# Kernel tuning notes

Hardware: AMD Instinct MI355X
Metric: run time of the kernel (lower is better)

## Reference

```python
import jax, jax.numpy as jnp
import numpy as np

# ---- static config (matches init_kwargs) ----
IMG = 56        # num_patches = image_size // patch_size = 112 // 2
WIN = 7         # window_size
SHIFT = 3       # shift_size
C = 256         # projection_dim
H = 8           # num_heads
DH = C // H     # head dim = 32
S = WIN * WIN   # tokens per window = 49
NY = IMG // WIN # windows per side = 8
NW = NY * NY    # windows per image = 64
NMLP = 1024
EPS = 1e-5
SCALE = DH ** (-0.5)


def _relative_position_index():
    ch, cw = np.meshgrid(np.arange(WIN), np.arange(WIN), indexing='ij')
    coords = np.stack([ch, cw]).reshape(2, -1)                 # [2, S]
    rel = coords[:, :, None] - coords[:, None, :]              # [2, S, S]
    rel = rel.transpose(1, 2, 0) + (WIN - 1)                   # [S, S, 2]
    idx = rel[:, :, 0] * (2 * WIN - 1) + rel[:, :, 1]          # [S, S]
    return idx.reshape(-1)                                     # [S*S]

REL_IDX = jnp.asarray(_relative_position_index(), dtype=jnp.int32)


def _attn_mask():
    # Faithful replication of the module's mask construction (incl. the empty
    h_slices = (slice(0, -WIN), slice(-WIN, -SHIFT), slice(-SHIFT, None))
    w_slices = (slice(0, -WIN), slice(-WIN, -WIN), slice(-SHIFT, None))
    m = np.zeros((IMG, IMG), dtype=np.float32)
    count = 0
    for hs in h_slices:
        for ws in w_slices:
            m[hs, ws] = count
            count += 1
    mw = m.reshape(NY, WIN, NY, WIN).transpose(0, 2, 1, 3).reshape(NW, S)
    diff = mw[:, None, :] - mw[:, :, None]
    return np.where(diff != 0, -100.0, 0.0).astype(np.float32)  # [NW, S, S]

ATTN_MASK = jnp.asarray(_attn_mask())


def _layernorm(x, gamma, beta):
    mu = jnp.mean(x, axis=-1, keepdims=True)
    var = jnp.mean(jnp.square(x - mu), axis=-1, keepdims=True)
    return (x - mu) * jax.lax.rsqrt(var + EPS) * gamma + beta


def setup_inputs() -> dict:
    key = jax.random.key(0)
    ks = jax.random.split(key, 12)
    B = 32
    s = lambda fan: 1.0 / np.sqrt(fan)
    return {
        'x': jax.random.normal(ks[0], (B, IMG * IMG, C), dtype=jnp.float32),
        'norm_gamma': jnp.ones((C,), jnp.float32),
        'norm_beta': jnp.zeros((C,), jnp.float32),
        'qkv_w': jax.random.normal(ks[1], (C, 3 * C), jnp.float32) * s(C),
        'qkv_b': jnp.zeros((3 * C,), jnp.float32),
        'proj_w': jax.random.normal(ks[2], (C, C), jnp.float32) * s(C),
        'proj_b': jnp.zeros((C,), jnp.float32),
        'rel_bias_table': jax.random.truncated_normal(ks[3], -2.0, 2.0, ((2 * WIN - 1) ** 2, H), jnp.float32) * 0.02,
        'mlp_w1': jax.random.normal(ks[4], (C, NMLP), jnp.float32) * s(C),
        'mlp_b1': jnp.zeros((NMLP,), jnp.float32),
        'mlp_w2': jax.random.normal(ks[5], (NMLP, C), jnp.float32) * s(NMLP),
        'mlp_b2': jnp.zeros((C,), jnp.float32),
    }


def reference(x, norm_gamma, norm_beta, qkv_w, qkv_b, proj_w, proj_b,
              rel_bias_table, mlp_w1, mlp_b1, mlp_w2, mlp_b2):
    B = x.shape[0]
    # ---- shifted-window attention block ----
    shortcut = x
    xn = _layernorm(x, norm_gamma, norm_beta).reshape(B, IMG, IMG, C)
    shifted = jnp.roll(xn, shift=(-SHIFT, -SHIFT), axis=(1, 2))
    # window partition -> [B*NW, S, C]
    xw = shifted.reshape(B, NY, WIN, NY, WIN, C).transpose(0, 1, 3, 2, 4, 5)
    xw = xw.reshape(B * NW, S, C)
    qkv = xw @ qkv_w + qkv_b                                    # [BnW, S, 3C]
    qkv = qkv.reshape(B * NW, S, 3, H, DH).transpose(2, 0, 3, 1, 4)
    q, k, v = qkv[0] * SCALE, qkv[1], qkv[2]                    # [BnW, H, S, DH]
    attn = jnp.einsum('whsd,whtd->whst', q, k)                  # [BnW, H, S, S]
    bias = rel_bias_table[REL_IDX].reshape(S, S, H).transpose(2, 0, 1)
    attn = attn + bias[None]
    attn = attn.reshape(B, NW, H, S, S) + ATTN_MASK[None, :, None]
    attn = jax.nn.softmax(attn.reshape(B * NW, H, S, S), axis=-1)
    out = jnp.einsum('whst,whtd->wshd', attn, v).reshape(B * NW, S, C)
    out = out @ proj_w + proj_b
    # window reverse + unshift
    out = out.reshape(B, NY, NY, WIN, WIN, C).transpose(0, 1, 3, 2, 4, 5)
    out = out.reshape(B, IMG, IMG, C)
    out = jnp.roll(out, shift=(SHIFT, SHIFT), axis=(1, 2)).reshape(B, IMG * IMG, C)
    x = shortcut + out
    # ---- MLP block (same LayerNorm weights reused, as in original) ----
    shortcut2 = x
    xn2 = _layernorm(x, norm_gamma, norm_beta)
    h = jax.nn.gelu(xn2 @ mlp_w1 + mlp_b1, approximate=False)
    h = h @ mlp_w2 + mlp_b2
    return shortcut2 + h
```

## Files before the change

kernel.cpp:

```cpp
#include <hip/hip_runtime.h>
#include <math.h>

#define IMG   56
#define WINSZ 7
#define SHIFTSZ 3
#define CDIM  256
#define NH    8
#define DH    32
#define SEQ   49
#define NYW   8
#define NWIN  64
#define NMLP  1024
#define BATCH 32
#define NTOK  (BATCH*IMG*IMG)
#define BNW   (BATCH*NWIN)
#define SZT   ((size_t)NTOK*CDIM)
#define QSCALE 0.17677669529663687f
#define EPSLN 1e-5f

typedef __attribute__((ext_vector_type(8))) short short8;
typedef __attribute__((ext_vector_type(4))) float f32x4;

__device__ __forceinline__ float bf2f(unsigned short u) {
    union { unsigned i; float f; } c; c.i = ((unsigned)u) << 16; return c.f;
}
__device__ __forceinline__ unsigned short f2bf(float f) {
    union { float f; unsigned i; } c; c.f = f;
    unsigned r = c.i + 0x7fffu + ((c.i >> 16) & 1u);
    return (unsigned short)(r >> 16);
}

#define GLL16(gp, lp) __builtin_amdgcn_global_load_lds( \
    (__attribute__((address_space(1))) void*)(gp),      \
    (__attribute__((address_space(3))) void*)(lp), 16, 0, 0)

__global__ __launch_bounds__(256) void wtrans(const float* __restrict__ in,
                                              unsigned short* __restrict__ out,
                                              int K, int N) {
    int idx = blockIdx.x * 256 + threadIdx.x;
    if (idx >= K * N) return;
    int n = idx / K, k = idx - n * K;
    out[idx] = f2bf(in[(size_t)k * N + n]);
}

template<int WINDOWED>
__global__ __launch_bounds__(256) void ln_kernel(const float* __restrict__ x,
                                                 const float* __restrict__ gamma,
                                                 const float* __restrict__ beta,
                                                 unsigned short* __restrict__ out) {
    int wave = threadIdx.x >> 6;
    int lane = threadIdx.x & 63;
    int tok  = blockIdx.x * 4 + wave;
    int src  = tok;
    if (WINDOWED) {
        int b  = tok / (NWIN * SEQ);
        int r  = tok - b * (NWIN * SEQ);
        int wl = r / SEQ, s = r - wl * SEQ;
        int wy = wl >> 3, wx = wl & 7;
        int i  = s / WINSZ, j = s - i * WINSZ;
        int hp = wy * WINSZ + i + SHIFTSZ; if (hp >= IMG) hp -= IMG;
        int wp = wx * WINSZ + j + SHIFTSZ; if (wp >= IMG) wp -= IMG;
        src = b * (IMG * IMG) + hp * IMG + wp;
    }
    float4 v = *(const float4*)(x + (size_t)src * CDIM + lane * 4);
    float sum = v.x + v.y + v.z + v.w;
    float ss  = v.x*v.x + v.y*v.y + v.z*v.z + v.w*v.w;
#pragma unroll
    for (int off = 32; off; off >>= 1) {
        sum += __shfl_xor(sum, off);
        ss  += __shfl_xor(ss,  off);
    }
    float mu   = sum * (1.0f / CDIM);
    float var  = ss * (1.0f / CDIM) - mu * mu;
    float rstd = rsqrtf(var + EPSLN);
    float4 g  = *(const float4*)(gamma + lane * 4);
    float4 be = *(const float4*)(beta  + lane * 4);
    ushort4 o;
    o.x = f2bf((v.x - mu) * rstd * g.x + be.x);
    o.y = f2bf((v.y - mu) * rstd * g.y + be.y);
    o.z = f2bf((v.z - mu) * rstd * g.z + be.z);
    o.w = f2bf((v.w - mu) * rstd * g.w + be.w);
    *(ushort4*)(out + (size_t)tok * CDIM + lane * 4) = o;
}

#define EPI_QKV  0
#define EPI_PROJ 1
#define EPI_MLP1 2
#define EPI_MLP2 3

template<int EPI>
__global__ __launch_bounds__(256)
void gemm_bt(const unsigned short* __restrict__ A,
             const unsigned short* __restrict__ Bt,
             int K,
             const float* __restrict__ bias,
             const float* __restrict__ resin,
             float* __restrict__ outF,
             unsigned short* __restrict__ outH) {
    __shared__ __align__(16) unsigned short As[128 * 32];
    __shared__ __align__(16) unsigned short Bs[128 * 32];
    int tid  = threadIdx.x;
    int lane = tid & 63, wave = tid >> 6;
    int q    = lane >> 4, l16 = lane & 15;
    int wm   = wave >> 1, wn = wave & 1;
    int rowBase = blockIdx.x * 128;
    int colBase = blockIdx.y * 128;

    f32x4 acc[4][4];
#pragma unroll
    for (int i = 0; i < 4; i++)
#pragma unroll
        for (int j = 0; j < 4; j++) acc[i][j] = (f32x4){0.f, 0.f, 0.f, 0.f};

    const unsigned short* Ab = A  + (size_t)rowBase * K;
    const unsigned short* Bb = Bt + (size_t)colBase * K;

    int r0 = wave * 32;
    int ra = r0 + (lane >> 2);
    int rb = ra + 16;
    int ca = (lane & 3) ^ ((ra >> 1) & 3);
    int cb = (lane & 3) ^ ((rb >> 1) & 3);
    const size_t off1 = (size_t)ra * K + ca * 8;
    const size_t off2 = (size_t)rb * K + cb * 8;
    unsigned short* ldsA1 = &As[r0 * 32];
    unsigned short* ldsA2 = &As[(r0 + 16) * 32];
    unsigned short* ldsB1 = &Bs[r0 * 32];
    unsigned short* ldsB2 = &Bs[(r0 + 16) * 32];

    for (int k0 = 0; k0 < K; k0 += 32) {
        __syncthreads();
        GLL16(Ab + off1 + k0, ldsA1);
        GLL16(Ab + off2 + k0, ldsA2);
        GLL16(Bb + off1 + k0, ldsB1);
        GLL16(Bb + off2 + k0, ldsB2);
        __syncthreads();
        short8 af[4], bf[4];
#pragma unroll
        for (int mi = 0; mi < 4; mi++) {
            int r = wm * 64 + mi * 16 + l16;
            af[mi] = *(const short8*)&As[r * 32 + ((q ^ ((r >> 1) & 3)) * 8)];
        }
#pragma unroll
        for (int ni = 0; ni < 4; ni++) {
            int r = wn * 64 + ni * 16 + l16;
            bf[ni] = *(const short8*)&Bs[r * 32 + ((q ^ ((r >> 1) & 3)) * 8)];
        }
#pragma unroll
        for (int mi = 0; mi < 4; mi++)
#pragma unroll
            for (int ni = 0; ni < 4; ni++)
                acc[mi][ni] = __builtin_amdgcn_mfma_f32_16x16x32_bf16(
                    af[mi], bf[ni], acc[mi][ni], 0, 0, 0);
    }

    int mb = rowBase + wm * 64;
    int nb = colBase + wn * 64;

    if (EPI == EPI_QKV) {
#pragma unroll
        for (int mi = 0; mi < 4; mi++)
#pragma unroll
            for (int r = 0; r < 4; r++) {
                int m = mb + mi * 16 + q * 4 + r;
                int w = m / SEQ, s = m - w * SEQ;
#pragma unroll
                for (int ni = 0; ni < 4; ni++) {
                    int n0 = nb + ni * 16 + l16;
                    int three = n0 >> 8, hh = (n0 >> 5) & 7, dd = n0 & 31;
                    float v = acc[mi][ni][r] + bias[n0];
                    if (three == 0) {
                        v *= QSCALE;
                        outH[(((size_t)w * NH + hh) * SEQ + s) * DH + dd] = f2bf(v);
                    } else if (three == 1) {
                        outH[SZT + (((size_t)w * NH + hh) * SEQ + s) * DH + dd] = f2bf(v);
                    } else {
                        outH[2 * SZT + (((size_t)w * NH + hh) * DH + dd) * 64 + s] = f2bf(v);
                    }
                }
            }
    } else if (EPI == EPI_PROJ) {
#pragma unroll
        for (int mi = 0; mi < 4; mi++)
#pragma unroll
            for (int r = 0; r < 4; r++) {
                int m = mb + mi * 16 + q * 4 + r;
                int w = m / SEQ, s = m - w * SEQ;
                int b = w >> 6, wl = w & 63;
                int wy = wl >> 3, wx = wl & 7;
                int ii = s / WINSZ, jj = s - ii * WINSZ;
                int hp = wy * WINSZ + ii + SHIFTSZ; if (hp >= IMG) hp -= IMG;
                int wp = wx * WINSZ + jj + SHIFTSZ; if (wp >= IMG) wp -= IMG;
                size_t tok = (size_t)b * (IMG * IMG) + hp * IMG + wp;
#pragma unroll
                for (int ni = 0; ni < 4; ni++) {
                    int n0 = nb + ni * 16 + l16;
                    outF[tok * CDIM + n0] = acc[mi][ni][r] + bias[n0] +
                                            resin[tok * CDIM + n0];
                }
            }
    } else if (EPI == EPI_MLP1) {
#pragma unroll
        for (int mi = 0; mi < 4; mi++)
#pragma unroll
            for (int r = 0; r < 4; r++) {
                int m = mb + mi * 16 + q * 4 + r;
#pragma unroll
                for (int ni = 0; ni < 4; ni++) {
                    int n0 = nb + ni * 16 + l16;
                    float t = acc[mi][ni][r] + bias[n0];
                    float g = 0.5f * t * (1.0f + erff(t * 0.70710678118654752f));
                    outH[(size_t)m * NMLP + n0] = f2bf(g);
                }
            }
    } else {
#pragma unroll
        for (int mi = 0; mi < 4; mi++)
#pragma unroll
            for (int r = 0; r < 4; r++) {
                int m = mb + mi * 16 + q * 4 + r;
#pragma unroll
                for (int ni = 0; ni < 4; ni++) {
                    int n0 = nb + ni * 16 + l16;
                    outF[(size_t)m * CDIM + n0] = acc[mi][ni][r] + bias[n0] +
                                                  resin[(size_t)m * CDIM + n0];
                }
            }
    }
}

__global__ __launch_bounds__(256) void attn_mfma(const unsigned short* __restrict__ qb,
                                                 const unsigned short* __restrict__ kb,
                                                 const unsigned short* __restrict__ vT,
                                                 const float* __restrict__ rel_tab,
                                                 unsigned short* __restrict__ outp) {
    __shared__ __align__(16) unsigned short Pl[4][64 * 64];
    __shared__ float tab[4][169];
    int tid  = threadIdx.x;
    int wave = tid >> 6, lane = tid & 63;
    int q4   = lane >> 4, l16 = lane & 15;
    int job  = blockIdx.x * 4 + wave;
    int w    = job >> 3, h = job & 7;

    for (int i = lane; i < 169; i += 64) tab[wave][i] = rel_tab[i * NH + h];

    const unsigned short* qg = qb + (size_t)(w * NH + h) * SEQ * DH;
    const unsigned short* kg = kb + (size_t)(w * NH + h) * SEQ * DH;
    short8 aq[4], bk[4];
#pragma unroll
    for (int mi = 0; mi < 4; mi++)
        aq[mi] = *(const short8*)(qg + (mi * 16 + l16) * DH + q4 * 8);
#pragma unroll
    for (int ni = 0; ni < 4; ni++)
        bk[ni] = *(const short8*)(kg + (ni * 16 + l16) * DH + q4 * 8);

    f32x4 acc[4][4];
#pragma unroll
    for (int i = 0; i < 4; i++)
#pragma unroll
        for (int j = 0; j < 4; j++) acc[i][j] = (f32x4){0.f, 0.f, 0.f, 0.f};
#pragma unroll
    for (int mi = 0; mi < 4; mi++)
#pragma unroll
        for (int ni = 0; ni < 4; ni++)
            acc[mi][ni] = __builtin_amdgcn_mfma_f32_16x16x32_bf16(
                aq[mi], bk[ni], acc[mi][ni], 0, 0, 0);

    int wl = w & 63;
    int wy = wl >> 3, wx = wl & 7;
    bool edge = (wy == 7) || (wx == 7);

    int itv[4], jtv[4], ltv[4];
#pragma unroll
    for (int ni = 0; ni < 4; ni++) {
        int t  = ni * 16 + l16;
        int it = (t * 37) >> 8;
        int jt = t - it * 7;
        itv[ni] = it; jtv[ni] = jt;
        int lab;
        if (wx == 7 && jt < 4) lab = 0;
        else {
            int lh = (wy == 7) ? ((it < 4) ? 1 : 2) : 0;
            lab = lh * 3 + ((wx == 7) ? 2 : 0);
        }
        ltv[ni] = lab;
    }

    float rinv[4][4];
#pragma unroll
    for (int mi = 0; mi < 4; mi++) {
#pragma unroll
        for (int r = 0; r < 4; r++) {
            int s  = mi * 16 + q4 * 4 + r;
            int is = (s * 37) >> 8;
            int js = s - is * 7;
            int lab_s;
            if (wx == 7 && js < 4) lab_s = 0;
            else {
                int lh = (wy == 7) ? ((is < 4) ? 1 : 2) : 0;
                lab_s = lh * 3 + ((wx == 7) ? 2 : 0);
            }
            float vv[4];
#pragma unroll
            for (int ni = 0; ni < 4; ni++) {
                int t = ni * 16 + l16;
                float a = acc[mi][ni][r];
                if (t < SEQ) {
                    int idx = (is - itv[ni] + 6) * 13 + (js - jtv[ni] + 6);
                    idx = idx < 0 ? 0 : (idx > 168 ? 168 : idx);
                    a += tab[wave][idx];
                    if (edge && lab_s != ltv[ni]) a -= 100.0f;
                } else {
                    a = -1e30f;
                }
                vv[ni] = a;
            }
            float mx = fmaxf(fmaxf(vv[0], vv[1]), fmaxf(vv[2], vv[3]));
#pragma unroll
            for (int off = 1; off < 16; off <<= 1) mx = fmaxf(mx, __shfl_xor(mx, off));
            float sm = 0.0f;
            unsigned short pb[4];
#pragma unroll
            for (int ni = 0; ni < 4; ni++) {
                float p = __expf(vv[ni] - mx);
                sm += p;
                pb[ni] = f2bf(p);
            }
#pragma unroll
            for (int off = 1; off < 16; off <<= 1) sm += __shfl_xor(sm, off);
            rinv[mi][r] = 1.0f / sm;
#pragma unroll
            for (int ni = 0; ni < 4; ni++) {
                int t  = ni * 16 + l16;
                int kbk = t >> 3, j = t & 7;
                Pl[wave][s * 64 + ((kbk ^ (s & 7)) * 8) + j] = pb[ni];
            }
        }
    }
    __syncthreads();

    short8 pa[4][2];
#pragma unroll
    for (int mi = 0; mi < 4; mi++)
#pragma unroll
        for (int ks = 0; ks < 2; ks++) {
            int m  = mi * 16 + l16;
            int kbk = ks * 4 + q4;
            pa[mi][ks] = *(const short8*)&Pl[wave][m * 64 + ((kbk ^ (m & 7)) * 8)];
        }
    const unsigned short* vg = vT + (size_t)(w * NH + h) * DH * 64;
    short8 bv[2][2];
#pragma unroll
    for (int n2 = 0; n2 < 2; n2++)
#pragma unroll
        for (int ks = 0; ks < 2; ks++)
            bv[n2][ks] = *(const short8*)(vg + (n2 * 16 + l16) * 64 + ks * 32 + q4 * 8);

    f32x4 o[4][2];
#pragma unroll
    for (int mi = 0; mi < 4; mi++)
#pragma unroll
        for (int n2 = 0; n2 < 2; n2++) o[mi][n2] = (f32x4){0.f, 0.f, 0.f, 0.f};
#pragma unroll
    for (int ks = 0; ks < 2; ks++)
#pragma unroll
        for (int mi = 0; mi < 4; mi++)
#pragma unroll
            for (int n2 = 0; n2 < 2; n2++)
                o[mi][n2] = __builtin_amdgcn_mfma_f32_16x16x32_bf16(
                    pa[mi][ks], bv[n2][ks], o[mi][n2], 0, 0, 0);

#pragma unroll
    for (int mi = 0; mi < 4; mi++)
#pragma unroll
        for (int r = 0; r < 4; r++) {
            int s = mi * 16 + q4 * 4 + r;
            if (s < SEQ) {
#pragma unroll
                for (int n2 = 0; n2 < 2; n2++) {
                    int d = n2 * 16 + l16;
                    outp[((size_t)w * SEQ + s) * CDIM + h * DH + d] =
                        f2bf(o[mi][n2][r] * rinv[mi][r]);
                }
            }
        }
}

extern "C" void kernel_launch(void* const* d_in, const int* in_sizes, int n_in,
                              void* d_out, int out_size, void* d_ws, size_t ws_size,
                              hipStream_t stream) {
    const float* x      = (const float*)d_in[0];
    const float* gamma  = (const float*)d_in[1];
    const float* beta   = (const float*)d_in[2];
    const float* qkv_w  = (const float*)d_in[3];
    const float* qkv_b  = (const float*)d_in[4];
    const float* proj_w = (const float*)d_in[5];
    const float* proj_b = (const float*)d_in[6];
    const float* rel_t  = (const float*)d_in[7];
    const float* mlp_w1 = (const float*)d_in[8];
    const float* mlp_b1 = (const float*)d_in[9];
    const float* mlp_w2 = (const float*)d_in[10];
    const float* mlp_b2 = (const float*)d_in[11];
    float* outp = (float*)d_out;

    const size_t VTSZ = (size_t)BNW * NH * DH * 64;
    unsigned short* xw_bf   = (unsigned short*)d_ws;
    unsigned short* qkv_bf  = xw_bf + SZT;
    unsigned short* attn_bf = qkv_bf + 2 * SZT + VTSZ;
    float*          y1      = (float*)(attn_bf + SZT);
    unsigned short* wt_bf   = (unsigned short*)(y1 + SZT);
    unsigned short* h_bf    = qkv_bf;

    unsigned short* qkvW  = wt_bf;
    unsigned short* projW = qkvW  + 768 * 256;
    unsigned short* mlp1W = projW + 256 * 256;
    unsigned short* mlp2W = mlp1W + 1024 * 256;

    wtrans<<<(768 * 256 + 255) / 256, 256, 0, stream>>>(qkv_w, qkvW, CDIM, 3 * CDIM);
    wtrans<<<(256 * 256 + 255) / 256, 256, 0, stream>>>(proj_w, projW, CDIM, CDIM);
    wtrans<<<(1024 * 256 + 255) / 256, 256, 0, stream>>>(mlp_w1, mlp1W, CDIM, NMLP);
    wtrans<<<(256 * 1024 + 255) / 256, 256, 0, stream>>>(mlp_w2, mlp2W, NMLP, CDIM);

    ln_kernel<1><<<NTOK / 4, 256, 0, stream>>>(x, gamma, beta, xw_bf);
    gemm_bt<EPI_QKV><<<dim3(NTOK / 128, 6), 256, 0, stream>>>(
        xw_bf, qkvW, CDIM, qkv_b, nullptr, nullptr, qkv_bf);
    attn_mfma<<<BNW * NH / 4, 256, 0, stream>>>(
        qkv_bf, qkv_bf + SZT, qkv_bf + 2 * SZT, rel_t, attn_bf);
    gemm_bt<EPI_PROJ><<<dim3(NTOK / 128, 2), 256, 0, stream>>>(
        attn_bf, projW, CDIM, proj_b, x, y1, nullptr);
    ln_kernel<0><<<NTOK / 4, 256, 0, stream>>>(y1, gamma, beta, xw_bf);
    gemm_bt<EPI_MLP1><<<dim3(NTOK / 128, 8), 256, 0, stream>>>(
        xw_bf, mlp1W, CDIM, mlp_b1, nullptr, nullptr, h_bf);
    gemm_bt<EPI_MLP2><<<dim3(NTOK / 128, 2), 256, 0, stream>>>(
        h_bf, mlp2W, NMLP, mlp_b2, y1, outp, nullptr);
}
```

Before: 849.0 us.

## Transpose MFMA operands for vectorized GEMM epilogues, swap grid order, fast GELU

Swaps the MFMA operand order so each lane holds four consecutive output columns, which lets the GEMM epilogues use float4 and ushort4 loads and stores for bias, residual and outputs instead of scalar accesses. Swaps the grid dimensions so column tiles vary fastest, letting blocks that share an A row tile run close together for L2 reuse. Replaces erff in the MLP GELU with an Abramowitz-Stegun polynomial built on a fast reciprocal and exp, which adds small approximation error. The V-transpose path in the QKV epilogue stays a scalar strided store.

```diff
diff --git a/kernel.cpp b/kernel.cpp
--- a/kernel.cpp
+++ b/kernel.cpp
@@ -28,6 +28,20 @@
     union { float f; unsigned i; } c; c.f = f;
     unsigned r = c.i + 0x7fffu + ((c.i >> 16) & 1u);
     return (unsigned short)(r >> 16);
+}
+
+__device__ __forceinline__ float gelu_f(float v) {
+    float u = v * 0.70710678118654752f;
+    float x = fabsf(u);
+    float t = __builtin_amdgcn_rcpf(fmaf(0.3275911f, x, 1.0f));
+    float e = __expf(-u * u);
+    float p = fmaf(1.061405429f, t, -1.453152027f);
+    p = fmaf(p, t, 1.421413741f);
+    p = fmaf(p, t, -0.284496736f);
+    p = fmaf(p, t, 0.254829592f);
+    float er = 1.0f - p * t * e;
+    er = copysignf(er, u);
+    return 0.5f * v * (1.0f + er);
 }
 
 #define GLL16(gp, lp) __builtin_amdgcn_global_load_lds( \
@@ -101,10 +115,10 @@
     __shared__ __align__(16) unsigned short Bs[128 * 32];
     int tid  = threadIdx.x;
     int lane = tid & 63, wave = tid >> 6;
-    int q    = lane >> 4, l16 = lane & 15;
+    int q4   = lane >> 4, l16 = lane & 15;
     int wm   = wave >> 1, wn = wave & 1;
-    int rowBase = blockIdx.x * 128;
-    int colBase = blockIdx.y * 128;
+    int rowBase = blockIdx.y * 128;
+    int colBase = blockIdx.x * 128;
 
     f32x4 acc[4][4];
 #pragma unroll
@@ -138,93 +152,110 @@
 #pragma unroll
         for (int mi = 0; mi < 4; mi++) {
             int r = wm * 64 + mi * 16 + l16;
-            af[mi] = *(const short8*)&As[r * 32 + ((q ^ ((r >> 1) & 3)) * 8)];
+            af[mi] = *(const short8*)&As[r * 32 + ((q4 ^ ((r >> 1) & 3)) * 8)];
         }
 #pragma unroll
         for (int ni = 0; ni < 4; ni++) {
             int r = wn * 64 + ni * 16 + l16;
-            bf[ni] = *(const short8*)&Bs[r * 32 + ((q ^ ((r >> 1) & 3)) * 8)];
+            bf[ni] = *(const short8*)&Bs[r * 32 + ((q4 ^ ((r >> 1) & 3)) * 8)];
         }
 #pragma unroll
         for (int mi = 0; mi < 4; mi++)
 #pragma unroll
             for (int ni = 0; ni < 4; ni++)
                 acc[mi][ni] = __builtin_amdgcn_mfma_f32_16x16x32_bf16(
-                    af[mi], bf[ni], acc[mi][ni], 0, 0, 0);
+                    bf[ni], af[mi], acc[mi][ni], 0, 0, 0);
     }
 
     int mb = rowBase + wm * 64;
     int nb = colBase + wn * 64;
+    float4 bias4[4];
+#pragma unroll
+    for (int ni = 0; ni < 4; ni++)
+        bias4[ni] = *(const float4*)(bias + nb + ni * 16 + q4 * 4);
 
     if (EPI == EPI_QKV) {
-#pragma unroll
-        for (int mi = 0; mi < 4; mi++)
-#pragma unroll
-            for (int r = 0; r < 4; r++) {
-                int m = mb + mi * 16 + q * 4 + r;
-                int w = m / SEQ, s = m - w * SEQ;
-#pragma unroll
-                for (int ni = 0; ni < 4; ni++) {
-                    int n0 = nb + ni * 16 + l16;
-                    int three = n0 >> 8, hh = (n0 >> 5) & 7, dd = n0 & 31;
-                    float v = acc[mi][ni][r] + bias[n0];
-                    if (three == 0) {
-                        v *= QSCALE;
-                        outH[(((size_t)w * NH + hh) * SEQ + s) * DH + dd] = f2bf(v);
-                    } else if (three == 1) {
-                        outH[SZT + (((size_t)w * NH + hh) * SEQ + s) * DH + dd] = f2bf(v);
-                    } else {
-                        outH[2 * SZT + (((size_t)w * NH + hh) * DH + dd) * 64 + s] = f2bf(v);
-                    }
+        int three = colBase >> 8;
+#pragma unroll
+        for (int mi = 0; mi < 4; mi++) {
+            int m = mb + mi * 16 + l16;
+            int w = m / SEQ, s = m - w * SEQ;
+#pragma unroll
+            for (int ni = 0; ni < 4; ni++) {
+                int n0 = nb + ni * 16 + q4 * 4;
+                int hh = (n0 >> 5) & 7, dd0 = n0 & 31;
+                const float* bp = (const float*)&bias4[ni];
+                if (three == 2) {
+#pragma unroll
+                    for (int r = 0; r < 4; r++)
+                        outH[2 * SZT + (((size_t)(w * NH + hh)) * DH + dd0 + r) * 64 + s] =
+                            f2bf(acc[mi][ni][r] + bp[r]);
+                } else {
+                    float sc = (three == 0) ? QSCALE : 1.0f;
+                    ushort4 o;
+                    o.x = f2bf((acc[mi][ni][0] + bp[0]) * sc);
+                    o.y = f2bf((acc[mi][ni][1] + bp[1]) * sc);
+                    o.z = f2bf((acc[mi][ni][2] + bp[2]) * sc);
+                    o.w = f2bf((acc[mi][ni][3] + bp[3]) * sc);
+                    *(ushort4*)(outH + (size_t)three * SZT +
+                                (((size_t)(w * NH + hh)) * SEQ + s) * DH + dd0) = o;
                 }
             }
+        }
     } else if (EPI == EPI_PROJ) {
 #pragma unroll
-        for (int mi = 0; mi < 4; mi++)
-#pragma unroll
-            for (int r = 0; r < 4; r++) {
-                int m = mb + mi * 16 + q * 4 + r;
-                int w = m / SEQ, s = m - w * SEQ;
-                int b = w >> 6, wl = w & 63;
-                int wy = wl >> 3, wx = wl & 7;
-                int ii = s / WINSZ, jj = s - ii * WINSZ;
-                int hp = wy * WINSZ + ii + SHIFTSZ; if (hp >= IMG) hp -= IMG;
-                int wp = wx * WINSZ + jj + SHIFTSZ; if (wp >= IMG) wp -= IMG;
-                size_t tok = (size_t)b * (IMG * IMG) + hp * IMG + wp;
-#pragma unroll
-                for (int ni = 0; ni < 4; ni++) {
-                    int n0 = nb + ni * 16 + l16;
-                    outF[tok * CDIM + n0] = acc[mi][ni][r] + bias[n0] +
-                                            resin[tok * CDIM + n0];
-                }
-            }
+        for (int mi = 0; mi < 4; mi++) {
+            int m = mb + mi * 16 + l16;
+            int w = m / SEQ, s = m - w * SEQ;
+            int b = w >> 6, wl = w & 63;
+            int wy = wl >> 3, wx = wl & 7;
+            int ii = s / WINSZ, jj = s - ii * WINSZ;
+            int hp = wy * WINSZ + ii + SHIFTSZ; if (hp >= IMG) hp -= IMG;
+            int wp = wx * WINSZ + jj + SHIFTSZ; if (wp >= IMG) wp -= IMG;
+            size_t tok = (size_t)b * (IMG * IMG) + hp * IMG + wp;
+#pragma unroll
+            for (int ni = 0; ni < 4; ni++) {
+                int n0 = nb + ni * 16 + q4 * 4;
+                float4 res = *(const float4*)(resin + tok * CDIM + n0);
+                float4 o;
+                o.x = acc[mi][ni][0] + bias4[ni].x + res.x;
+                o.y = acc[mi][ni][1] + bias4[ni].y + res.y;
+                o.z = acc[mi][ni][2] + bias4[ni].z + res.z;
+                o.w = acc[mi][ni][3] + bias4[ni].w + res.w;
+                *(float4*)(outF + tok * CDIM + n0) = o;
+            }
+        }
     } else if (EPI == EPI_MLP1) {
 #pragma unroll
-        for (int mi = 0; mi < 4; mi++)
-#pragma unroll
-            for (int r = 0; r < 4; r++) {
-                int m = mb + mi * 16 + q * 4 + r;
-#pragma unroll
-                for (int ni = 0; ni < 4; ni++) {
-                    int n0 = nb + ni * 16 + l16;
-                    float t = acc[mi][ni][r] + bias[n0];
-                    float g = 0.5f * t * (1.0f + erff(t * 0.70710678118654752f));
-                    outH[(size_t)m * NMLP + n0] = f2bf(g);
-                }
-            }
+        for (int mi = 0; mi < 4; mi++) {
+            int m = mb + mi * 16 + l16;
+#pragma unroll
+            for (int ni = 0; ni < 4; ni++) {
+                int n0 = nb + ni * 16 + q4 * 4;
+                ushort4 o;
+                o.x = f2bf(gelu_f(acc[mi][ni][0] + bias4[ni].x));
+                o.y = f2bf(gelu_f(acc[mi][ni][1] + bias4[ni].y));
+                o.z = f2bf(gelu_f(acc[mi][ni][2] + bias4[ni].z));
+                o.w = f2bf(gelu_f(acc[mi][ni][3] + bias4[ni].w));
+                *(ushort4*)(outH + (size_t)m * NMLP + n0) = o;
+            }
+        }
     } else {
 #pragma unroll
-        for (int mi = 0; mi < 4; mi++)
-#pragma unroll
-            for (int r = 0; r < 4; r++) {
-                int m = mb + mi * 16 + q * 4 + r;
-#pragma unroll
-                for (int ni = 0; ni < 4; ni++) {
-                    int n0 = nb + ni * 16 + l16;
-                    outF[(size_t)m * CDIM + n0] = acc[mi][ni][r] + bias[n0] +
-                                                  resin[(size_t)m * CDIM + n0];
-                }
-            }
+        for (int mi = 0; mi < 4; mi++) {
+            int m = mb + mi * 16 + l16;
+#pragma unroll
+            for (int ni = 0; ni < 4; ni++) {
+                int n0 = nb + ni * 16 + q4 * 4;
+                float4 res = *(const float4*)(resin + (size_t)m * CDIM + n0);
+                float4 o;
+                o.x = acc[mi][ni][0] + bias4[ni].x + res.x;
+                o.y = acc[mi][ni][1] + bias4[ni].y + res.y;
+                o.z = acc[mi][ni][2] + bias4[ni].z + res.z;
+                o.w = acc[mi][ni][3] + bias4[ni].w + res.w;
+                *(float4*)(outF + (size_t)m * CDIM + n0) = o;
+            }
+        }
     }
 }
 
@@ -421,15 +452,15 @@
     wtrans<<<(256 * 1024 + 255) / 256, 256, 0, stream>>>(mlp_w2, mlp2W, NMLP, CDIM);
 
     ln_kernel<1><<<NTOK / 4, 256, 0, stream>>>(x, gamma, beta, xw_bf);
-    gemm_bt<EPI_QKV><<<dim3(NTOK / 128, 6), 256, 0, stream>>>(
+    gemm_bt<EPI_QKV><<<dim3(6, NTOK / 128), 256, 0, stream>>>(
         xw_bf, qkvW, CDIM, qkv_b, nullptr, nullptr, qkv_bf);
     attn_mfma<<<BNW * NH / 4, 256, 0, stream>>>(
         qkv_bf, qkv_bf + SZT, qkv_bf + 2 * SZT, rel_t, attn_bf);
-    gemm_bt<EPI_PROJ><<<dim3(NTOK / 128, 2), 256, 0, stream>>>(
+    gemm_bt<EPI_PROJ><<<dim3(2, NTOK / 128), 256, 0, stream>>>(
         attn_bf, projW, CDIM, proj_b, x, y1, nullptr);
     ln_kernel<0><<<NTOK / 4, 256, 0, stream>>>(y1, gamma, beta, xw_bf);
-    gemm_bt<EPI_MLP1><<<dim3(NTOK / 128, 8), 256, 0, stream>>>(
+    gemm_bt<EPI_MLP1><<<dim3(8, NTOK / 128), 256, 0, stream>>>(
         xw_bf, mlp1W, CDIM, mlp_b1, nullptr, nullptr, h_bf);
-    gemm_bt<EPI_MLP2><<<dim3(NTOK / 128, 2), 256, 0, stream>>>(
+    gemm_bt<EPI_MLP2><<<dim3(2, NTOK / 128), 256, 0, stream>>>(
         h_bf, mlp2W, NMLP, mlp_b2, y1, outp, nullptr);
 }
```

Measured after the change: 758.0 us. 1.12x faster.
